# Performance work log

Hardware: AMD Instinct MI355X
Metric: run time of the kernel (lower is better)

The kernel has to match this reference:

```python
import jax, jax.numpy as jnp
import numpy as np

D_MODEL = 1024
H = 16
D_K = D_MODEL // H


def setup_inputs() -> dict:
    key = jax.random.key(0)
    ks = jax.random.split(key, 9)
    s = 0.02
    x = jax.random.normal(ks[0], (2, 2048, D_MODEL), dtype=jnp.float32)
    Wq = jax.random.normal(ks[1], (D_MODEL, D_MODEL), dtype=jnp.float32) * s
    bq = jax.random.normal(ks[2], (D_MODEL,), dtype=jnp.float32) * s
    Wk = jax.random.normal(ks[3], (D_MODEL, D_MODEL), dtype=jnp.float32) * s
    bk = jax.random.normal(ks[4], (D_MODEL,), dtype=jnp.float32) * s
    Wv = jax.random.normal(ks[5], (D_MODEL, D_MODEL), dtype=jnp.float32) * s
    bv = jax.random.normal(ks[6], (D_MODEL,), dtype=jnp.float32) * s
    Wo = jax.random.normal(ks[7], (D_MODEL, D_MODEL), dtype=jnp.float32) * s
    bo = jax.random.normal(ks[8], (D_MODEL,), dtype=jnp.float32) * s
    return {"x": x, "Wq": Wq, "bq": bq, "Wk": Wk, "bk": bk,
            "Wv": Wv, "bv": bv, "Wo": Wo, "bo": bo}


def reference(x, Wq, bq, Wk, bk, Wv, bv, Wo, bo):
    b, s, _ = x.shape
    scale = 1.0 / jnp.sqrt(jnp.float32(D_K))
    # projections; [b, s, d] -> [b, h, s, d_k]
    def split_heads(t):
        return t.reshape(b, s, H, D_K).transpose(0, 2, 1, 3)
    q = split_heads(x @ Wq + bq)
    k = split_heads(x @ Wk + bk)
    v = split_heads(x @ Wv + bv)
    scores = jnp.einsum('bhqd,bhkd->bhqk', q, k) * scale  # [b,h,s,s]
    attn = jax.nn.softmax(scores, axis=-1)
    ctx = jnp.einsum('bhqk,bhkd->bhqd', attn, v)
    ctx = ctx.transpose(0, 2, 1, 3).reshape(b, s, D_MODEL)
    return ctx @ Wo + bo + x
```

## Files before the change

### kernel.cpp

```cpp
#include <hip/hip_runtime.h>
#include <hip/hip_bf16.h>
#include <stdint.h>

#define D_MODEL 1024
#define NH 16
#define DK 64
#define S_LEN 2048

typedef __attribute__((ext_vector_type(8))) __bf16 bf16x8;
typedef __attribute__((ext_vector_type(4))) float f32x4;

#define GLOBAL_AS __attribute__((address_space(1)))
#define LDS_AS    __attribute__((address_space(3)))

__device__ __forceinline__ void async16(const ushort* g, ushort* l) {
    __builtin_amdgcn_global_load_lds(
        (const GLOBAL_AS uint32_t*)(uintptr_t)(const void*)g,
        (LDS_AS uint32_t*)(uint32_t)(uintptr_t)(void*)l,
        16, 0, 0);
}

template <int N>
__device__ __forceinline__ void pipe_barrier() {
    asm volatile("s_waitcnt vmcnt(%0)\n\ts_barrier" :: "n"(N) : "memory");
}

__device__ __forceinline__ float fast_exp2(float x) {
    float r;
    asm("v_exp_f32 %0, %1" : "=v"(r) : "v"(x));
    return r;
}

__device__ __forceinline__ ushort f2bf(float f) {
    union { float f; uint32_t u; } v; v.f = f;
    uint32_t lsb = (v.u >> 16) & 1u;
    return (ushort)((v.u + 0x7fffu + lsb) >> 16);
}

__device__ __forceinline__ uint32_t packbf(float a, float b) {
    union { float f; uint32_t u; } x, y; x.f = a; y.f = b;
    return ((x.u + 0x8000u) >> 16) | ((y.u + 0x8000u) & 0xffff0000u);
}

__device__ __forceinline__ bf16x8 ldfrag(const ushort* p) {
    union { uint4 u; bf16x8 b; } cv;
    cv.u = *(const uint4*)p;
    return cv.b;
}


__global__ void cvt_x_kernel(const float* __restrict__ x, ushort* __restrict__ xb) {
    int i = blockIdx.x * 256 + threadIdx.x;
    float4 v = ((const float4*)x)[i];
    ushort4 o;
    o.x = f2bf(v.x); o.y = f2bf(v.y); o.z = f2bf(v.z); o.w = f2bf(v.w);
    ((ushort4*)xb)[i] = o;
}

__global__ void transpose_cvt4_kernel(
    const float* __restrict__ W0, const float* __restrict__ W1,
    const float* __restrict__ W2, const float* __restrict__ W3,
    ushort* __restrict__ D0, ushort* __restrict__ D1,
    ushort* __restrict__ D2, ushort* __restrict__ D3) {
    const float* W; ushort* D;
    switch (blockIdx.z) {
        case 0: W = W0; D = D0; break;
        case 1: W = W1; D = D1; break;
        case 2: W = W2; D = D2; break;
        default: W = W3; D = D3; break;
    }
    __shared__ float tile[32][33];
    int bx = blockIdx.x * 32, by = blockIdx.y * 32;
    int tx = threadIdx.x, ty = threadIdx.y;
#pragma unroll
    for (int j = 0; j < 32; j += 8)
        tile[ty + j][tx] = W[(size_t)(by + ty + j) * D_MODEL + bx + tx];
    __syncthreads();
#pragma unroll
    for (int j = 0; j < 32; j += 8)
        D[(size_t)(bx + ty + j) * D_MODEL + by + tx] = f2bf(tile[tx][ty + j]);
}

__global__ void cvt_bias_kernel(const float* __restrict__ bq, const float* __restrict__ bk,
                                const float* __restrict__ bv, float* __restrict__ out) {
    int i = blockIdx.x * 256 + threadIdx.x;
    float v = (i < 1024) ? bq[i] : (i < 2048 ? bk[i - 1024] : bv[i - 2048]);
    out[i] = v;
}

template <int MODE>
__global__ __launch_bounds__(256) void gemm_kernel(
    const ushort* __restrict__ A, const ushort* __restrict__ Bt,
    const float* __restrict__ bias,
    ushort* __restrict__ outQ, ushort* __restrict__ outK, ushort* __restrict__ outVt,
    const float* __restrict__ xres, float* __restrict__ outF) {
    constexpr int BN = (MODE == 0) ? 128 : 64;
    constexpr int NI = (MODE == 0) ? 4 : 2;
    constexpr int NS = (MODE == 0) ? 4 : 3;
    constexpr int ABUF = 4096;
    constexpr int BBUF = (MODE == 0) ? 4096 : 2048;
    constexpr int SMEM = (MODE == 0) ? 32768 : 24576;
    __shared__ __align__(16) ushort smem[SMEM];
    ushort* sAb = smem;
    ushort* sBb = smem + 4 * ABUF;

    const int tid = threadIdx.x;
    const int wave = tid >> 6, lane = tid & 63;
    const int lr = lane & 15, lq = lane >> 4;
    const int srow = lane >> 3, sp = lane & 7;

    const int bid = blockIdx.x;
    const int xcd = bid & 7, lb = bid >> 3;
    int bx, by;
    if (MODE == 0) { bx = xcd * 3 + (lb % 3); by = lb / 3; }
    else           { by = xcd * 4 + (lb & 3); bx = lb >> 2; }
    const int blockM = by * 128;
    const int blockN = bx * BN;
    const int waveM = (wave >> 1) * 64;
    const int waveN = (MODE == 0) ? (wave & 1) * 64 : (wave & 1) * 32;

    auto stage = [&](int k0, int buf) {
        ushort* a = sAb + buf * ABUF;
#pragma unroll
        for (int t = 0; t < 2; t++) {
            int Rb = wave * 16 + t * 8;
            int R = Rb + srow;
            int L = sp ^ (R & 7);
            int m = 2 * R + (L >> 2);
            int kc = L & 3;
            async16(&A[(size_t)(blockM + m) * D_MODEL + k0 + kc * 8], a + Rb * 64);
        }
        ushort* b = sBb + buf * BBUF;
        if (MODE == 0) {
#pragma unroll
            for (int t = 0; t < 2; t++) {
                int Rb = wave * 16 + t * 8;
                int R = Rb + srow;
                int L = sp ^ (R & 7);
                int n = 2 * R + (L >> 2);
                int kc = L & 3;
                async16(&Bt[(size_t)(blockN + n) * D_MODEL + k0 + kc * 8], b + Rb * 64);
            }
        } else {
            int Rb = wave * 8;
            int R = Rb + srow;
            int L = sp ^ (R & 7);
            int n = 2 * R + (L >> 2);
            int kc = L & 3;
            async16(&Bt[(size_t)(blockN + n) * D_MODEL + k0 + kc * 8], b + Rb * 64);
        }
    };

    const int RA = (waveM >> 1) + (lr >> 1);
    const int offA = RA * 64 + ((((lr & 1) * 4 + lq) ^ (RA & 7)) * 8);
    const int RB = (waveN >> 1) + (lr >> 1);
    const int offB = RB * 64 + ((((lr & 1) * 4 + lq) ^ (RB & 7)) * 8);

    f32x4 acc[4][NI] = {};

    stage(0, 0);
    stage(32, 1);
    stage(64, 2);
    pipe_barrier<2 * NS>();

#pragma unroll 4
    for (int k = 0; k < 32; k++) {
        const int buf = k & 3;
        if (k + 3 < 32) stage((k + 3) * 32, (k + 3) & 3);
        const ushort* a = sAb + buf * ABUF;
        const ushort* b = sBb + buf * BBUF;
        bf16x8 af[4], bfr[NI];
#pragma unroll
        for (int mi = 0; mi < 4; mi++)
            af[mi] = ldfrag(&a[offA + mi * 512]);
#pragma unroll
        for (int ni = 0; ni < NI; ni++)
            bfr[ni] = ldfrag(&b[offB + ni * 512]);
#pragma unroll
        for (int mi = 0; mi < 4; mi++)
#pragma unroll
            for (int ni = 0; ni < NI; ni++)
                acc[mi][ni] = __builtin_amdgcn_mfma_f32_16x16x32_bf16(
                    af[mi], bfr[ni], acc[mi][ni], 0, 0, 0);
        if (k < 30) pipe_barrier<2 * NS>();
        else if (k == 30) pipe_barrier<0>();
    }
    __syncthreads();

    const int bglob = blockM >> 11;
    const int sbase = blockM & 2047;

    if (MODE == 0) {
        const int which = bx >> 3;
        if (which < 2) {
            const float scale = (which == 0) ? 0.1803368801f : 1.0f;
#pragma unroll
            for (int ni = 0; ni < 4; ni++) {
                const int n_loc = waveN + ni * 16 + lr;
                const float bn = bias[blockN + n_loc];
#pragma unroll
                for (int mi = 0; mi < 4; mi++)
#pragma unroll
                    for (int r = 0; r < 4; r++) {
                        int m_loc = waveM + mi * 16 + lq * 4 + r;
                        smem[m_loc * 136 + n_loc] =
                            f2bf((acc[mi][ni][r] + bn) * scale);
                    }
            }
            __syncthreads();
            ushort* outp = (which == 0) ? outQ : outK;
            const int hbase = (which == 0) ? bx * 2 : (bx - 8) * 2;
#pragma unroll
            for (int j = 0; j < 8; j++) {
                int c = tid + j * 256;
                int m = c >> 4, nc = c & 15;
                int hh = nc >> 3, d8 = nc & 7;
                uint4 w = *(uint4*)&smem[m * 136 + nc * 8];
                size_t bh = (size_t)(bglob * NH + hbase + hh);
                *(uint4*)&outp[(bh * S_LEN + sbase + m) * DK + d8 * 8] = w;
            }
        } else {
#pragma unroll
            for (int ni = 0; ni < 4; ni++) {
                const int n_loc = waveN + ni * 16 + lr;
                const float bn = bias[blockN + n_loc];
#pragma unroll
                for (int mi = 0; mi < 4; mi++) {
                    uint2 w;
                    w.x = packbf(acc[mi][ni][0] + bn, acc[mi][ni][1] + bn);
                    w.y = packbf(acc[mi][ni][2] + bn, acc[mi][ni][3] + bn);
                    int m_base = waveM + mi * 16 + lq * 4;
                    *(uint2*)&smem[n_loc * 136 + m_base] = w;
                }
            }
            __syncthreads();
            const int hbase = (bx - 16) * 2;
#pragma unroll
            for (int j = 0; j < 8; j++) {
                int c = tid + j * 256;
                int n_loc = c >> 4, m8 = c & 15;
                int d = n_loc & 63, hh = n_loc >> 6;
                uint4 w = *(uint4*)&smem[n_loc * 136 + m8 * 8];
                size_t bh = (size_t)(bglob * NH + hbase + hh);
                *(uint4*)&outVt[(bh * DK + d) * S_LEN + sbase + m8 * 8] = w;
            }
        }
    } else {
        float* sCf = (float*)smem;
#pragma unroll
        for (int ni = 0; ni < 2; ni++) {
            const int n_loc = waveN + ni * 16 + lr;
            const float bn = bias[blockN + n_loc];
#pragma unroll
            for (int mi = 0; mi < 4; mi++)
#pragma unroll
                for (int r = 0; r < 4; r++) {
                    int m_loc = waveM + mi * 16 + lq * 4 + r;
                    sCf[m_loc * 68 + n_loc] = acc[mi][ni][r] + bn;
                }
        }
        __syncthreads();
#pragma unroll
        for (int j = 0; j < 8; j++) {
            int c = tid + j * 256;
            int m = c >> 4, nc = c & 15;
            float4 v = *(float4*)&sCf[m * 68 + nc * 4];
            size_t idx = (size_t)(blockM + m) * D_MODEL + blockN + nc * 4;
            float4 xr = *(const float4*)&xres[idx];
            v.x += xr.x; v.y += xr.y; v.z += xr.z; v.w += xr.w;
            *(float4*)&outF[idx] = v;
        }
    }
}

__global__ __launch_bounds__(256, 2) void attn_kernel(
    const ushort* __restrict__ Q, const ushort* __restrict__ Km,
    const ushort* __restrict__ Vt, ushort* __restrict__ ctx) {
    const int bid = blockIdx.x;
    const int xcd = bid & 7, lb = bid >> 3;
    const int bh = xcd * 4 + (lb & 3);
    const int qt = lb >> 2;
    const int q0 = qt * 128;
    __shared__ __align__(16) ushort sK[3][64 * 64];
    __shared__ __align__(16) ushort sV[3][64 * 64];
    __shared__ __align__(16) ushort sQP[4][32 * 64];
    const int tid = threadIdx.x;
    const int wave = tid >> 6, lane = tid & 63;
    const int lr = lane & 15, lq = lane >> 4;
    const int srow = lane >> 3, sp = lane & 7;
    const ushort* Qh = Q + (size_t)bh * S_LEN * DK;
    const ushort* Kh = Km + (size_t)bh * S_LEN * DK;
    const ushort* Vh = Vt + (size_t)bh * DK * S_LEN;
    ushort* sPw = sQP[wave];

#pragma unroll
    for (int t = 0; t < 4; t++) {
        int row = t * 8 + srow;
        int c = sp ^ (row & 7);
        async16(&Qh[(size_t)(q0 + wave * 32 + row) * DK + c * 8],
                &sPw[t * 8 * 64]);
    }

    auto stageKV = [&](int k0, int buf) {
#pragma unroll
        for (int t = 0; t < 2; t++) {
            int row = wave * 16 + t * 8 + srow;
            int c = sp ^ (row & 7);
            async16(&Kh[(size_t)(k0 + row) * DK + c * 8],
                    &sK[buf][(wave * 16 + t * 8) * 64]);
            async16(&Vh[(size_t)row * S_LEN + k0 + c * 8],
                    &sV[buf][(wave * 16 + t * 8) * 64]);
        }
    };

    stageKV(0, 0);
    stageKV(64, 1);
    __syncthreads();

    bf16x8 qf[2][2];
#pragma unroll
    for (int nj = 0; nj < 2; nj++)
#pragma unroll
        for (int kk = 0; kk < 2; kk++)
            qf[nj][kk] = ldfrag(&sPw[(nj * 16 + lr) * 64 +
                                     (((kk * 4 + lq) ^ (lr & 7)) * 8)]);

    union { uint4 u; bf16x8 b; } one_u;
    one_u.u = make_uint4(0x3F803F80u, 0x3F803F80u, 0x3F803F80u, 0x3F803F80u);
    const bf16x8 ones = one_u.b;

    f32x4 cacc[2][4] = {};
    f32x4 ssum[2] = {};

    int cur = 0;
    for (int k = 0; k < 32; k++) {
        int nx = cur + 2; if (nx >= 3) nx -= 3;
        if (k + 2 < 32) stageKV((k + 2) * 64, nx);
        const ushort* sk = sK[cur];
        const ushort* sv = sV[cur];

        f32x4 sacc[4][2] = {};
#pragma unroll
        for (int kk = 0; kk < 2; kk++) {
            bf16x8 kf[4];
            int swz = ((kk * 4 + lq) ^ (lr & 7)) * 8;
#pragma unroll
            for (int mi = 0; mi < 4; mi++)
                kf[mi] = ldfrag(&sk[(mi * 16 + lr) * 64 + swz]);
#pragma unroll
            for (int mi = 0; mi < 4; mi++)
#pragma unroll
                for (int nj = 0; nj < 2; nj++)
                    sacc[mi][nj] = __builtin_amdgcn_mfma_f32_16x16x32_bf16(
                        kf[mi], qf[nj][kk], sacc[mi][nj], 0, 0, 0);
        }

#pragma unroll
        for (int mi = 0; mi < 4; mi++)
#pragma unroll
            for (int nj = 0; nj < 2; nj++) {
                float p0 = fast_exp2(sacc[mi][nj][0]);
                float p1 = fast_exp2(sacc[mi][nj][1]);
                float p2 = fast_exp2(sacc[mi][nj][2]);
                float p3 = fast_exp2(sacc[mi][nj][3]);
                uint2 w;
                w.x = packbf(p0, p1);
                w.y = packbf(p2, p3);
                int physc = (mi * 2 + (lq >> 1)) ^ (lr & 7);
                *(uint2*)&sPw[(nj * 16 + lr) * 64 + physc * 8 + (lq & 1) * 4] = w;
            }

#pragma unroll
        for (int ks = 0; ks < 2; ks++) {
            bf16x8 pf[2], vf[4];
            int swz = ((ks * 4 + lq) ^ (lr & 7)) * 8;
#pragma unroll
            for (int nj = 0; nj < 2; nj++)
                pf[nj] = ldfrag(&sPw[(nj * 16 + lr) * 64 + swz]);
#pragma unroll
            for (int nd = 0; nd < 4; nd++)
                vf[nd] = ldfrag(&sv[(nd * 16 + lr) * 64 + swz]);
#pragma unroll
            for (int nj = 0; nj < 2; nj++)
#pragma unroll
                for (int nd = 0; nd < 4; nd++)
                    cacc[nj][nd] = __builtin_amdgcn_mfma_f32_16x16x32_bf16(
                        pf[nj], vf[nd], cacc[nj][nd], 0, 0, 0);
#pragma unroll
            for (int nj = 0; nj < 2; nj++)
                ssum[nj] = __builtin_amdgcn_mfma_f32_16x16x32_bf16(
                    pf[nj], ones, ssum[nj], 0, 0, 0);
        }

        if (k < 30) pipe_barrier<4>();
        else if (k == 30) pipe_barrier<0>();
        cur = (cur == 2) ? 0 : cur + 1;
    }

    const int b = bh >> 4, h = bh & 15;
    float inv[2][4];
#pragma unroll
    for (int nj = 0; nj < 2; nj++)
#pragma unroll
        for (int r = 0; r < 4; r++)
            inv[nj][r] = __builtin_amdgcn_rcpf(ssum[nj][r]);
#pragma unroll
    for (int nj = 0; nj < 2; nj++)
#pragma unroll
        for (int nd = 0; nd < 4; nd++)
#pragma unroll
            for (int r = 0; r < 4; r++) {
                int qrow = q0 + wave * 32 + nj * 16 + lq * 4 + r;
                int d = nd * 16 + lr;
                float v = cacc[nj][nd][r] * inv[nj][r];
                ctx[(size_t)(b * S_LEN + qrow) * D_MODEL + h * DK + d] = f2bf(v);
            }
}


extern "C" void kernel_launch(void* const* d_in, const int* in_sizes, int n_in,
                              void* d_out, int out_size, void* d_ws, size_t ws_size,
                              hipStream_t stream) {
    const float* x  = (const float*)d_in[0];
    const float* Wq = (const float*)d_in[1];
    const float* bq = (const float*)d_in[2];
    const float* Wk = (const float*)d_in[3];
    const float* bk = (const float*)d_in[4];
    const float* Wv = (const float*)d_in[5];
    const float* bv = (const float*)d_in[6];
    const float* Wo = (const float*)d_in[7];
    const float* bo = (const float*)d_in[8];

    char* ws = (char*)d_ws;
    ushort* xb    = (ushort*)(ws);
    ushort* wqkv  = (ushort*)(ws + (8ull  << 20));
    ushort* wo_t  = (ushort*)(ws + (14ull << 20));
    ushort* qbuf  = (ushort*)(ws + (16ull << 20));
    ushort* kbuf  = (ushort*)(ws + (24ull << 20));
    ushort* vtb   = (ushort*)(ws + (32ull << 20));
    ushort* ctx   = (ushort*)(ws + (40ull << 20));
    float*  biasq = (float*)(ws + (48ull << 20));

    cvt_x_kernel<<<4096, 256, 0, stream>>>(x, xb);
    transpose_cvt4_kernel<<<dim3(32, 32, 4), dim3(32, 8), 0, stream>>>(
        Wq, Wk, Wv, Wo, wqkv, wqkv + 1024 * 1024, wqkv + 2 * 1024 * 1024, wo_t);
    cvt_bias_kernel<<<12, 256, 0, stream>>>(bq, bk, bv, biasq);

    gemm_kernel<0><<<768, 256, 0, stream>>>(
        xb, wqkv, biasq, qbuf, kbuf, vtb, nullptr, nullptr);
    attn_kernel<<<512, 256, 0, stream>>>(qbuf, kbuf, vtb, ctx);
    gemm_kernel<1><<<512, 256, 0, stream>>>(
        ctx, wo_t, bo, nullptr, nullptr, nullptr, x, (float*)d_out);
}
```

Measured before the change: 206.9 us.

## Double attention query tile per wave and compute row sums with scalar adds

Each wave now processes 64 query rows instead of 32, so each block covers 256 queries and the grid is halved. Each K/V tile loaded into LDS is reused across twice as many queries. The K/V staging drops from triple to double buffering with a full wait each iteration. The ones-vector MFMA that built the softmax denominator is replaced by per-lane float adds followed by a cross-lane shuffle reduction. In exchange, register pressure rises (launch bounds relaxed to 1 block per SM), there are only 256 blocks, which risks underfilling the GPU, and there is less load/compute overlap.

```diff
diff --git a/kernel.cpp b/kernel.cpp
--- a/kernel.cpp
+++ b/kernel.cpp
@@ -273,17 +273,17 @@
     }
 }
 
-__global__ __launch_bounds__(256, 2) void attn_kernel(
+__global__ __launch_bounds__(256, 1) void attn_kernel(
     const ushort* __restrict__ Q, const ushort* __restrict__ Km,
     const ushort* __restrict__ Vt, ushort* __restrict__ ctx) {
     const int bid = blockIdx.x;
     const int xcd = bid & 7, lb = bid >> 3;
     const int bh = xcd * 4 + (lb & 3);
     const int qt = lb >> 2;
-    const int q0 = qt * 128;
-    __shared__ __align__(16) ushort sK[3][64 * 64];
-    __shared__ __align__(16) ushort sV[3][64 * 64];
-    __shared__ __align__(16) ushort sQP[4][32 * 64];
+    const int q0 = qt * 256;
+    __shared__ __align__(16) ushort sK[2][64 * 64];
+    __shared__ __align__(16) ushort sV[2][64 * 64];
+    __shared__ __align__(16) ushort sQP[4][64 * 64];
     const int tid = threadIdx.x;
     const int wave = tid >> 6, lane = tid & 63;
     const int lr = lane & 15, lq = lane >> 4;
@@ -294,10 +294,10 @@
     ushort* sPw = sQP[wave];
 
 #pragma unroll
-    for (int t = 0; t < 4; t++) {
+    for (int t = 0; t < 8; t++) {
         int row = t * 8 + srow;
         int c = sp ^ (row & 7);
-        async16(&Qh[(size_t)(q0 + wave * 32 + row) * DK + c * 8],
+        async16(&Qh[(size_t)(q0 + wave * 64 + row) * DK + c * 8],
                 &sPw[t * 8 * 64]);
     }
 
@@ -314,32 +314,26 @@
     };
 
     stageKV(0, 0);
-    stageKV(64, 1);
     __syncthreads();
 
-    bf16x8 qf[2][2];
-#pragma unroll
-    for (int nj = 0; nj < 2; nj++)
+    bf16x8 qf[4][2];
+#pragma unroll
+    for (int nj = 0; nj < 4; nj++)
 #pragma unroll
         for (int kk = 0; kk < 2; kk++)
             qf[nj][kk] = ldfrag(&sPw[(nj * 16 + lr) * 64 +
                                      (((kk * 4 + lq) ^ (lr & 7)) * 8)]);
 
-    union { uint4 u; bf16x8 b; } one_u;
-    one_u.u = make_uint4(0x3F803F80u, 0x3F803F80u, 0x3F803F80u, 0x3F803F80u);
-    const bf16x8 ones = one_u.b;
-
-    f32x4 cacc[2][4] = {};
-    f32x4 ssum[2] = {};
-
-    int cur = 0;
+    f32x4 cacc[4][4] = {};
+    float lsum[4] = {0.f, 0.f, 0.f, 0.f};
+
     for (int k = 0; k < 32; k++) {
-        int nx = cur + 2; if (nx >= 3) nx -= 3;
-        if (k + 2 < 32) stageKV((k + 2) * 64, nx);
-        const ushort* sk = sK[cur];
-        const ushort* sv = sV[cur];
-
-        f32x4 sacc[4][2] = {};
+        const int buf = k & 1;
+        if (k + 1 < 32) stageKV((k + 1) * 64, buf ^ 1);
+        const ushort* sk = sK[buf];
+        const ushort* sv = sV[buf];
+
+        f32x4 sacc[4][4] = {};
 #pragma unroll
         for (int kk = 0; kk < 2; kk++) {
             bf16x8 kf[4];
@@ -350,7 +344,7 @@
 #pragma unroll
             for (int mi = 0; mi < 4; mi++)
 #pragma unroll
-                for (int nj = 0; nj < 2; nj++)
+                for (int nj = 0; nj < 4; nj++)
                     sacc[mi][nj] = __builtin_amdgcn_mfma_f32_16x16x32_bf16(
                         kf[mi], qf[nj][kk], sacc[mi][nj], 0, 0, 0);
         }
@@ -358,11 +352,12 @@
 #pragma unroll
         for (int mi = 0; mi < 4; mi++)
 #pragma unroll
-            for (int nj = 0; nj < 2; nj++) {
+            for (int nj = 0; nj < 4; nj++) {
                 float p0 = fast_exp2(sacc[mi][nj][0]);
                 float p1 = fast_exp2(sacc[mi][nj][1]);
                 float p2 = fast_exp2(sacc[mi][nj][2]);
                 float p3 = fast_exp2(sacc[mi][nj][3]);
+                lsum[nj] += (p0 + p1) + (p2 + p3);
                 uint2 w;
                 w.x = packbf(p0, p1);
                 w.y = packbf(p2, p3);
@@ -372,47 +367,50 @@
 
 #pragma unroll
         for (int ks = 0; ks < 2; ks++) {
-            bf16x8 pf[2], vf[4];
+            bf16x8 pf[4], vf[4];
             int swz = ((ks * 4 + lq) ^ (lr & 7)) * 8;
 #pragma unroll
-            for (int nj = 0; nj < 2; nj++)
+            for (int nj = 0; nj < 4; nj++)
                 pf[nj] = ldfrag(&sPw[(nj * 16 + lr) * 64 + swz]);
 #pragma unroll
             for (int nd = 0; nd < 4; nd++)
                 vf[nd] = ldfrag(&sv[(nd * 16 + lr) * 64 + swz]);
 #pragma unroll
-            for (int nj = 0; nj < 2; nj++)
+            for (int nj = 0; nj < 4; nj++)
 #pragma unroll
                 for (int nd = 0; nd < 4; nd++)
                     cacc[nj][nd] = __builtin_amdgcn_mfma_f32_16x16x32_bf16(
                         pf[nj], vf[nd], cacc[nj][nd], 0, 0, 0);
-#pragma unroll
-            for (int nj = 0; nj < 2; nj++)
-                ssum[nj] = __builtin_amdgcn_mfma_f32_16x16x32_bf16(
-                    pf[nj], ones, ssum[nj], 0, 0, 0);
-        }
-
-        if (k < 30) pipe_barrier<4>();
-        else if (k == 30) pipe_barrier<0>();
-        cur = (cur == 2) ? 0 : cur + 1;
-    }
+        }
+
+        if (k < 31) pipe_barrier<0>();
+    }
+
+    float inv[4];
+#pragma unroll
+    for (int nj = 0; nj < 4; nj++) {
+        float l = lsum[nj];
+        l += __shfl_xor(l, 16);
+        l += __shfl_xor(l, 32);
+        inv[nj] = __builtin_amdgcn_rcpf(l);
+    }
+    float invr[4][4];
+#pragma unroll
+    for (int nj = 0; nj < 4; nj++)
+#pragma unroll
+        for (int r = 0; r < 4; r++)
+            invr[nj][r] = __shfl(inv[nj], lq * 4 + r);
 
     const int b = bh >> 4, h = bh & 15;
-    float inv[2][4];
-#pragma unroll
-    for (int nj = 0; nj < 2; nj++)
-#pragma unroll
-        for (int r = 0; r < 4; r++)
-            inv[nj][r] = __builtin_amdgcn_rcpf(ssum[nj][r]);
-#pragma unroll
-    for (int nj = 0; nj < 2; nj++)
+#pragma unroll
+    for (int nj = 0; nj < 4; nj++)
 #pragma unroll
         for (int nd = 0; nd < 4; nd++)
 #pragma unroll
             for (int r = 0; r < 4; r++) {
-                int qrow = q0 + wave * 32 + nj * 16 + lq * 4 + r;
+                int qrow = q0 + wave * 64 + nj * 16 + lq * 4 + r;
                 int d = nd * 16 + lr;
-                float v = cacc[nj][nd][r] * inv[nj][r];
+                float v = cacc[nj][nd][r] * invr[nj][r];
                 ctx[(size_t)(b * S_LEN + qrow) * D_MODEL + h * DK + d] = f2bf(v);
             }
 }
@@ -448,7 +446,7 @@
 
     gemm_kernel<0><<<768, 256, 0, stream>>>(
         xb, wqkv, biasq, qbuf, kbuf, vtb, nullptr, nullptr);
-    attn_kernel<<<512, 256, 0, stream>>>(qbuf, kbuf, vtb, ctx);
+    attn_kernel<<<256, 256, 0, stream>>>(qbuf, kbuf, vtb, ctx);
     gemm_kernel<1><<<512, 256, 0, stream>>>(
         ctx, wo_t, bo, nullptr, nullptr, nullptr, x, (float*)d_out);
 }
```

After: 217.4 us. +5.0%, slower.
